# Optimization experiments

Measured on AMD Instinct MI355X. Metric: run time of the kernel, lower is better.

## Reference

```python
import jax, jax.numpy as jnp
import numpy as np

B, T, H, D = 4, 1024, 16, 64


def setup_inputs() -> dict:
    key = jax.random.key(0)
    kq, kk, kwq, kwk = jax.random.split(key, 4)
    q = jax.random.normal(kq, (B, T, H, D), dtype=jnp.float32)
    k = jax.random.normal(kk, (B, T, H, D), dtype=jnp.float32)
    # HedgehogFeatureMap init: eye weight, zero bias; add small noise so grads flow
    Wq = jnp.eye(D, dtype=jnp.float32) + 0.02 * jax.random.normal(kwq, (D, D), dtype=jnp.float32)
    Wk = jnp.eye(D, dtype=jnp.float32) + 0.02 * jax.random.normal(kwk, (D, D), dtype=jnp.float32)
    bq = jnp.zeros((D,), dtype=jnp.float32)
    bk = jnp.zeros((D,), dtype=jnp.float32)
    return {"q": q, "k": k, "Wq": Wq, "bq": bq, "Wk": Wk, "bk": bk}


def _feature_map(x, W, b):
    # nn.Linear(head_dim, head_dim) then cat([exp(y), exp(-y)], -1) -> [..., 2D]
    y = jnp.einsum('bthd,ed->bthe', x, W) + b
    return jnp.concatenate([jnp.exp(y), jnp.exp(-y)], axis=-1)


def reference(q, k, Wq, bq, Wk, bk):
    # true softmax attention map: [B, T, H, T]
    scale = q.shape[-1] ** 0.5
    scores = jnp.einsum('bthd,bThd->bthT', q, k) / scale
    true_attn_map = jax.nn.softmax(scores, axis=-1)
    # predicted quadratic linear attention with hedgehog feature maps
    phi_q = _feature_map(q, Wq, bq)   # [B,T,H,2D]
    phi_k = _feature_map(k, Wk, bk)   # [B,T,H,2D]
    qk = jnp.einsum('bthd,bThd->bthT', phi_q, phi_k)
    pred_attn_map = qk / jnp.sum(qk, axis=-1, keepdims=True)
    return jnp.stack([true_attn_map, pred_attn_map])  # [2,B,T,H,T]
```

## Files before the change

### kernel.cpp

```cpp
#include <hip/hip_runtime.h>

typedef unsigned short u16;
typedef unsigned int u32;
typedef __attribute__((ext_vector_type(8))) short short8;
typedef __attribute__((ext_vector_type(4))) float floatx4;

#define MFMA16(A,B,C) __builtin_amdgcn_mfma_f32_16x16x32_bf16((A),(B),(C),0,0,0)


__device__ __forceinline__ u16 f2bf(float f){
  u32 u = __float_as_uint(f);
  u32 r = (u + 0x7fffu + ((u >> 16) & 1u)) >> 16;
  return (u16)r;
}
__device__ __forceinline__ float bf2f(u16 h){
  return __uint_as_float(((u32)h) << 16);
}
__device__ __forceinline__ short8 ld8(const u16* p){
  return *(const short8*)p;
}

__global__ __launch_bounds__(256) void featmap_kernel(
    const float* __restrict__ q, const float* __restrict__ k,
    const float* __restrict__ Wq, const float* __restrict__ bq,
    const float* __restrict__ Wk, const float* __restrict__ bk,
    u16* __restrict__ qh, u16* __restrict__ ql,
    u16* __restrict__ kh, u16* __restrict__ kl,
    u16* __restrict__ phiq, u16* __restrict__ phik) {
  u32 gid = blockIdx.x * 256u + threadIdx.x;
  bool is_k = gid >= 65536u;
  u32 r = is_k ? (gid - 65536u) : gid;
  const float* __restrict__ x = (is_k ? k : q) + (size_t)r * 64u;
  const float* __restrict__ W = is_k ? Wk : Wq;
  const float* __restrict__ bias = is_k ? bk : bq;
  u32 b = r >> 14, t = (r >> 4) & 1023u, h = r & 15u;
  u32 orow = (b * 16u + h) * 1024u + t;

  float xv[64];
#pragma unroll
  for (int i = 0; i < 16; i++) {
    float4 v = ((const float4*)x)[i];
    xv[4 * i + 0] = v.x; xv[4 * i + 1] = v.y;
    xv[4 * i + 2] = v.z; xv[4 * i + 3] = v.w;
  }

  float scale = is_k ? 1.0f : 0.125f;
  u16* hdst = (is_k ? kh : qh) + (size_t)orow * 64u;
  u16* ldst = (is_k ? kl : ql) + (size_t)orow * 64u;
#pragma unroll
  for (int c = 0; c < 8; c++) {
    u16 hi[8] __attribute__((aligned(16)));
    u16 lo[8] __attribute__((aligned(16)));
#pragma unroll
    for (int j = 0; j < 8; j++) {
      float xs = xv[c * 8 + j] * scale;
      u16 hb = f2bf(xs);
      hi[j] = hb;
      lo[j] = f2bf(xs - bf2f(hb));
    }
    ((uint4*)hdst)[c] = *(const uint4*)hi;
    ((uint4*)ldst)[c] = *(const uint4*)lo;
  }

  u16* pdst = (is_k ? phik : phiq) + (size_t)orow * 128u;
#pragma unroll
  for (int c = 0; c < 4; c++) {
    float accs[16];
#pragma unroll
    for (int i = 0; i < 16; i++) accs[i] = bias[c * 16 + i];
#pragma unroll
    for (int d = 0; d < 64; d++) {
      float xd = xv[d];
#pragma unroll
      for (int i = 0; i < 16; i++) accs[i] += xd * W[(c * 16 + i) * 64 + d];
    }
    u16 pl[16] __attribute__((aligned(16)));
    u16 pm[16] __attribute__((aligned(16)));
#pragma unroll
    for (int i = 0; i < 16; i++) {
      pl[i] = f2bf(__expf(accs[i]));
      pm[i] = f2bf(__expf(-accs[i]));
    }
    ((uint4*)pdst)[2 * c + 0] = ((const uint4*)pl)[0];
    ((uint4*)pdst)[2 * c + 1] = ((const uint4*)pl)[1];
    ((uint4*)(pdst + 64))[2 * c + 0] = ((const uint4*)pm)[0];
    ((uint4*)(pdst + 64))[2 * c + 1] = ((const uint4*)pm)[1];
  }
}

__global__ __launch_bounds__(128) void colsum_kernel(
    const u16* __restrict__ phik, float* __restrict__ colsum) {
  int bh = blockIdx.x;
  int e = threadIdx.x;
  const u16* p = phik + (size_t)bh * 1024u * 128u + e;
  float s = 0.f;
#pragma unroll 8
  for (int t = 0; t < 1024; t++) s += bf2f(p[(size_t)t * 128u]);
  colsum[bh * 128 + e] = s;
}

__global__ __launch_bounds__(256) void fused_kernel(
    const u16* __restrict__ qh, const u16* __restrict__ ql,
    const u16* __restrict__ kh, const u16* __restrict__ kl,
    const u16* __restrict__ phiq, const u16* __restrict__ phik,
    const float* __restrict__ colsum, float* __restrict__ out) {
  int bh = blockIdx.x >> 6, strip = blockIdx.x & 63;
  int tid = threadIdx.x, w = tid >> 6, lane = tid & 63, quad = lane >> 4, n16 = lane & 15;
  u32 base = (u32)bh * 1024u;

  __shared__ float cs[128];
  __shared__ float rzp_s[16];
  __shared__ float zb[4][16];

  if (tid < 128) cs[tid] = colsum[bh * 128 + tid];
  __syncthreads();

  {
    int row = tid >> 4, seg = tid & 15;
    u32 grow = base + strip * 16u + (u32)row;
    short8 v = ld8(phiq + (size_t)grow * 128u + seg * 8);
    float p = 0.f;
#pragma unroll
    for (int j = 0; j < 8; j++) p += bf2f((u16)v[j]) * cs[seg * 8 + j];
#pragma unroll
    for (int off = 1; off < 16; off <<= 1) p += __shfl_xor(p, off);
    if (seg == 0) rzp_s[row] = 1.f / p;
  }

  u32 qrow = base + strip * 16u + n16;
  short8 bqh[2], bql[2], bpq[4];
#pragma unroll
  for (int ks = 0; ks < 2; ks++) {
    bqh[ks] = ld8(qh + (size_t)qrow * 64u + ks * 32u + quad * 8u);
    bql[ks] = ld8(ql + (size_t)qrow * 64u + ks * 32u + quad * 8u);
  }
#pragma unroll
  for (int ks = 0; ks < 4; ks++)
    bpq[ks] = ld8(phiq + (size_t)qrow * 128u + ks * 32u + quad * 8u);

  __syncthreads();
  float rzp = rzp_s[n16];

  u32 bb = (u32)bh >> 4, hh = (u32)bh & 15u;
  u32 t = strip * 16u + n16;
  float* out0 = out + ((size_t)(bb * 1024u + t) * 16u + hh) * 1024u;
  float* out1 = out0 + 67108864u;

  float pt[64];
#pragma unroll
  for (int ct = 0; ct < 16; ct++) {
    u32 col = base + (u32)(w * 16 + ct) * 16u + n16;
    const u16* kp = kh + (size_t)col * 64u + quad * 8u;
    const u16* lp = kl + (size_t)col * 64u + quad * 8u;
    const u16* pp = phik + (size_t)col * 128u + quad * 8u;
    short8 b0 = ld8(kp), b1 = ld8(kp + 32), c0 = ld8(lp), c1 = ld8(lp + 32);
    short8 p0 = ld8(pp), p1 = ld8(pp + 32), p2 = ld8(pp + 64), p3 = ld8(pp + 96);
    floatx4 acc = {0.f, 0.f, 0.f, 0.f};
    acc = MFMA16(b0, bqh[0], acc);
    acc = MFMA16(b1, bqh[1], acc);
    acc = MFMA16(c0, bqh[0], acc);
    acc = MFMA16(c1, bqh[1], acc);
    acc = MFMA16(b0, bql[0], acc);
    acc = MFMA16(b1, bql[1], acc);
    floatx4 ap = {0.f, 0.f, 0.f, 0.f};
    ap = MFMA16(p0, bpq[0], ap);
    ap = MFMA16(p1, bpq[1], ap);
    ap = MFMA16(p2, bpq[2], ap);
    ap = MFMA16(p3, bpq[3], ap);
#pragma unroll
    for (int r = 0; r < 4; r++) pt[ct * 4 + r] = __expf(acc[r]);
    float4 ov;
    ov.x = ap[0] * rzp; ov.y = ap[1] * rzp;
    ov.z = ap[2] * rzp; ov.w = ap[3] * rzp;
    *(float4*)(out1 + (u32)(w * 16 + ct) * 16u + quad * 4u) = ov;
  }

  float s = 0.f;
#pragma unroll
  for (int i = 0; i < 64; i++) s += pt[i];
  s += __shfl_xor(s, 16);
  s += __shfl_xor(s, 32);
  if (lane < 16) zb[w][lane] = s;
  __syncthreads();
  float rzt = 1.f / (zb[0][n16] + zb[1][n16] + zb[2][n16] + zb[3][n16]);

#pragma unroll
  for (int ct = 0; ct < 16; ct++) {
    float4 ov;
    ov.x = pt[ct * 4 + 0] * rzt; ov.y = pt[ct * 4 + 1] * rzt;
    ov.z = pt[ct * 4 + 2] * rzt; ov.w = pt[ct * 4 + 3] * rzt;
    *(float4*)(out0 + (u32)(w * 16 + ct) * 16u + quad * 4u) = ov;
  }
}

extern "C" void kernel_launch(void* const* d_in, const int* in_sizes, int n_in,
                              void* d_out, int out_size, void* d_ws, size_t ws_size,
                              hipStream_t stream) {
  const float* q  = (const float*)d_in[0];
  const float* k  = (const float*)d_in[1];
  const float* Wq = (const float*)d_in[2];
  const float* bq = (const float*)d_in[3];
  const float* Wk = (const float*)d_in[4];
  const float* bk = (const float*)d_in[5];
  unsigned char* ws = (unsigned char*)d_ws;
  u16* qh   = (u16*)(ws + (0ull  << 20));
  u16* ql   = (u16*)(ws + (8ull  << 20));
  u16* kh   = (u16*)(ws + (16ull << 20));
  u16* kl   = (u16*)(ws + (24ull << 20));
  u16* phiq = (u16*)(ws + (32ull << 20));
  u16* phik = (u16*)(ws + (48ull << 20));
  float* colsum = (float*)(ws + (64ull << 20));
  float* out = (float*)d_out;

  hipLaunchKernelGGL(featmap_kernel, dim3(512), dim3(256), 0, stream,
                     q, k, Wq, bq, Wk, bk, qh, ql, kh, kl, phiq, phik);
  hipLaunchKernelGGL(colsum_kernel, dim3(64), dim3(128), 0, stream, phik, colsum);
  hipLaunchKernelGGL(fused_kernel, dim3(4096), dim3(256), 0, stream,
                     qh, ql, kh, kl, phiq, phik, colsum, out);
}
```

Measured before the change: 937.6 us.

## Widen fused blocks to 16 waves, split colsum with atomics, remap featmap rows

The fused kernel now runs 1024 threads per block, so each of 16 waves covers 4 column tiles instead of 16. This shrinks per-thread register arrays and spreads the row-softmax reduction over 16 waves. The colsum reduction is split across 8 chunks per head, combined with atomicAdd, with featmap zeroing the accumulator first. Featmap threads are remapped so consecutive threads write consecutive output rows rather than consecutive input rows. This trades strided input reads for contiguous workspace writes, and the larger blocks may lower occupancy flexibility.

```diff
diff --git a/kernel.cpp b/kernel.cpp
--- a/kernel.cpp
+++ b/kernel.cpp
@@ -26,15 +26,19 @@
     const float* __restrict__ Wk, const float* __restrict__ bk,
     u16* __restrict__ qh, u16* __restrict__ ql,
     u16* __restrict__ kh, u16* __restrict__ kl,
-    u16* __restrict__ phiq, u16* __restrict__ phik) {
+    u16* __restrict__ phiq, u16* __restrict__ phik,
+    float* __restrict__ colsum) {
   u32 gid = blockIdx.x * 256u + threadIdx.x;
+  if (gid < 8192u) colsum[gid] = 0.f;
   bool is_k = gid >= 65536u;
   u32 r = is_k ? (gid - 65536u) : gid;
-  const float* __restrict__ x = (is_k ? k : q) + (size_t)r * 64u;
+  u32 t = r & 1023u, bh = r >> 10;
+  u32 b = bh >> 4, h = bh & 15u;
+  const float* __restrict__ x =
+      (is_k ? k : q) + ((size_t)(b * 1024u + t) * 16u + h) * 64u;
   const float* __restrict__ W = is_k ? Wk : Wq;
   const float* __restrict__ bias = is_k ? bk : bq;
-  u32 b = r >> 14, t = (r >> 4) & 1023u, h = r & 15u;
-  u32 orow = (b * 16u + h) * 1024u + t;
+  u32 orow = bh * 1024u + t;
 
   float xv[64];
 #pragma unroll
@@ -90,16 +94,16 @@
 
 __global__ __launch_bounds__(128) void colsum_kernel(
     const u16* __restrict__ phik, float* __restrict__ colsum) {
-  int bh = blockIdx.x;
+  int bh = blockIdx.x >> 3, chunk = blockIdx.x & 7;
   int e = threadIdx.x;
-  const u16* p = phik + (size_t)bh * 1024u * 128u + e;
+  const u16* p = phik + (size_t)bh * 131072u + (size_t)chunk * 16384u + e;
   float s = 0.f;
 #pragma unroll 8
-  for (int t = 0; t < 1024; t++) s += bf2f(p[(size_t)t * 128u]);
-  colsum[bh * 128 + e] = s;
-}
-
-__global__ __launch_bounds__(256) void fused_kernel(
+  for (int t = 0; t < 128; t++) s += bf2f(p[(size_t)t * 128u]);
+  atomicAdd(&colsum[bh * 128 + e], s);
+}
+
+__global__ __launch_bounds__(1024) void fused_kernel(
     const u16* __restrict__ qh, const u16* __restrict__ ql,
     const u16* __restrict__ kh, const u16* __restrict__ kl,
     const u16* __restrict__ phiq, const u16* __restrict__ phik,
@@ -110,12 +114,12 @@
 
   __shared__ float cs[128];
   __shared__ float rzp_s[16];
-  __shared__ float zb[4][16];
+  __shared__ float zb[16][16];
 
   if (tid < 128) cs[tid] = colsum[bh * 128 + tid];
   __syncthreads();
 
-  {
+  if (tid < 256) {
     int row = tid >> 4, seg = tid & 15;
     u32 grow = base + strip * 16u + (u32)row;
     short8 v = ld8(phiq + (size_t)grow * 128u + seg * 8);
@@ -146,10 +150,11 @@
   float* out0 = out + ((size_t)(bb * 1024u + t) * 16u + hh) * 1024u;
   float* out1 = out0 + 67108864u;
 
-  float pt[64];
-#pragma unroll
-  for (int ct = 0; ct < 16; ct++) {
-    u32 col = base + (u32)(w * 16 + ct) * 16u + n16;
+  float pt[16];
+#pragma unroll
+  for (int ct = 0; ct < 4; ct++) {
+    u32 ctg = (u32)(w * 4 + ct);
+    u32 col = base + ctg * 16u + n16;
     const u16* kp = kh + (size_t)col * 64u + quad * 8u;
     const u16* lp = kl + (size_t)col * 64u + quad * 8u;
     const u16* pp = phik + (size_t)col * 128u + quad * 8u;
@@ -172,24 +177,28 @@
     float4 ov;
     ov.x = ap[0] * rzp; ov.y = ap[1] * rzp;
     ov.z = ap[2] * rzp; ov.w = ap[3] * rzp;
-    *(float4*)(out1 + (u32)(w * 16 + ct) * 16u + quad * 4u) = ov;
+    *(float4*)(out1 + ctg * 16u + quad * 4u) = ov;
   }
 
   float s = 0.f;
 #pragma unroll
-  for (int i = 0; i < 64; i++) s += pt[i];
+  for (int i = 0; i < 16; i++) s += pt[i];
   s += __shfl_xor(s, 16);
   s += __shfl_xor(s, 32);
   if (lane < 16) zb[w][lane] = s;
   __syncthreads();
-  float rzt = 1.f / (zb[0][n16] + zb[1][n16] + zb[2][n16] + zb[3][n16]);
-
-#pragma unroll
-  for (int ct = 0; ct < 16; ct++) {
+  float zt = 0.f;
+#pragma unroll
+  for (int w2 = 0; w2 < 16; w2++) zt += zb[w2][n16];
+  float rzt = 1.f / zt;
+
+#pragma unroll
+  for (int ct = 0; ct < 4; ct++) {
+    u32 ctg = (u32)(w * 4 + ct);
     float4 ov;
     ov.x = pt[ct * 4 + 0] * rzt; ov.y = pt[ct * 4 + 1] * rzt;
     ov.z = pt[ct * 4 + 2] * rzt; ov.w = pt[ct * 4 + 3] * rzt;
-    *(float4*)(out0 + (u32)(w * 16 + ct) * 16u + quad * 4u) = ov;
+    *(float4*)(out0 + ctg * 16u + quad * 4u) = ov;
   }
 }
 
@@ -213,8 +222,8 @@
   float* out = (float*)d_out;
 
   hipLaunchKernelGGL(featmap_kernel, dim3(512), dim3(256), 0, stream,
-                     q, k, Wq, bq, Wk, bk, qh, ql, kh, kl, phiq, phik);
-  hipLaunchKernelGGL(colsum_kernel, dim3(64), dim3(128), 0, stream, phik, colsum);
-  hipLaunchKernelGGL(fused_kernel, dim3(4096), dim3(256), 0, stream,
+                     q, k, Wq, bq, Wk, bk, qh, ql, kh, kl, phiq, phik, colsum);
+  hipLaunchKernelGGL(colsum_kernel, dim3(512), dim3(128), 0, stream, phik, colsum);
+  hipLaunchKernelGGL(fused_kernel, dim3(4096), dim3(1024), 0, stream,
                      qh, ql, kh, kl, phiq, phik, colsum, out);
 }
```

Result: no change. 936.5 us (-0.1%).

## Stage attention tiles in LDS for coalesced row writes and drop colsum kernel

Applied to the files above, without the earlier changes.

The feature-map kernel now writes intermediates in the original [B,T,H] row order instead of a permuted head-major layout. The fused kernel grows to 1024 threads and stages both score tiles (16 rows by 1024 cols) in shared memory. Each wave then reads a full row, reduces it with wave shuffles, and writes contiguous 4KB output rows. The separate colsum pass and its prediction denominator are replaced by a direct row-sum of the predicted scores. The cost is about 128KB of LDS per block, which limits occupancy to one block per CU, and the K/phi reads become strided because of the unpermuted layout.

```diff
diff --git a/kernel.cpp b/kernel.cpp
--- a/kernel.cpp
+++ b/kernel.cpp
@@ -33,8 +33,6 @@
   const float* __restrict__ x = (is_k ? k : q) + (size_t)r * 64u;
   const float* __restrict__ W = is_k ? Wk : Wq;
   const float* __restrict__ bias = is_k ? bk : bq;
-  u32 b = r >> 14, t = (r >> 4) & 1023u, h = r & 15u;
-  u32 orow = (b * 16u + h) * 1024u + t;
 
   float xv[64];
 #pragma unroll
@@ -45,8 +43,8 @@
   }
 
   float scale = is_k ? 1.0f : 0.125f;
-  u16* hdst = (is_k ? kh : qh) + (size_t)orow * 64u;
-  u16* ldst = (is_k ? kl : ql) + (size_t)orow * 64u;
+  u16* hdst = (is_k ? kh : qh) + (size_t)r * 64u;
+  u16* ldst = (is_k ? kl : ql) + (size_t)r * 64u;
 #pragma unroll
   for (int c = 0; c < 8; c++) {
     u16 hi[8] __attribute__((aligned(16)));
@@ -62,7 +60,7 @@
     ((uint4*)ldst)[c] = *(const uint4*)lo;
   }
 
-  u16* pdst = (is_k ? phik : phiq) + (size_t)orow * 128u;
+  u16* pdst = (is_k ? phik : phiq) + (size_t)r * 128u;
 #pragma unroll
   for (int c = 0; c < 4; c++) {
     float accs[16];
@@ -88,71 +86,38 @@
   }
 }
 
-__global__ __launch_bounds__(128) void colsum_kernel(
-    const u16* __restrict__ phik, float* __restrict__ colsum) {
-  int bh = blockIdx.x;
-  int e = threadIdx.x;
-  const u16* p = phik + (size_t)bh * 1024u * 128u + e;
-  float s = 0.f;
-#pragma unroll 8
-  for (int t = 0; t < 1024; t++) s += bf2f(p[(size_t)t * 128u]);
-  colsum[bh * 128 + e] = s;
-}
-
-__global__ __launch_bounds__(256) void fused_kernel(
+__global__ __launch_bounds__(1024) void fused_kernel(
     const u16* __restrict__ qh, const u16* __restrict__ ql,
     const u16* __restrict__ kh, const u16* __restrict__ kl,
     const u16* __restrict__ phiq, const u16* __restrict__ phik,
-    const float* __restrict__ colsum, float* __restrict__ out) {
+    float* __restrict__ out) {
   int bh = blockIdx.x >> 6, strip = blockIdx.x & 63;
   int tid = threadIdx.x, w = tid >> 6, lane = tid & 63, quad = lane >> 4, n16 = lane & 15;
-  u32 base = (u32)bh * 1024u;
-
-  __shared__ float cs[128];
-  __shared__ float rzp_s[16];
-  __shared__ float zb[4][16];
-
-  if (tid < 128) cs[tid] = colsum[bh * 128 + tid];
-  __syncthreads();
-
-  {
-    int row = tid >> 4, seg = tid & 15;
-    u32 grow = base + strip * 16u + (u32)row;
-    short8 v = ld8(phiq + (size_t)grow * 128u + seg * 8);
-    float p = 0.f;
-#pragma unroll
-    for (int j = 0; j < 8; j++) p += bf2f((u16)v[j]) * cs[seg * 8 + j];
-#pragma unroll
-    for (int off = 1; off < 16; off <<= 1) p += __shfl_xor(p, off);
-    if (seg == 0) rzp_s[row] = 1.f / p;
-  }
-
-  u32 qrow = base + strip * 16u + n16;
+  u32 b = (u32)bh >> 4, h = (u32)bh & 15u;
+
+  __shared__ float smT[16][1028];
+  __shared__ float smP[16][1028];
+
+  u32 tq = (u32)strip * 16u + (u32)n16;
+  size_t Rq = (size_t)((b * 1024u + tq) * 16u + h);
   short8 bqh[2], bql[2], bpq[4];
 #pragma unroll
   for (int ks = 0; ks < 2; ks++) {
-    bqh[ks] = ld8(qh + (size_t)qrow * 64u + ks * 32u + quad * 8u);
-    bql[ks] = ld8(ql + (size_t)qrow * 64u + ks * 32u + quad * 8u);
+    bqh[ks] = ld8(qh + Rq * 64u + ks * 32 + quad * 8);
+    bql[ks] = ld8(ql + Rq * 64u + ks * 32 + quad * 8);
   }
 #pragma unroll
   for (int ks = 0; ks < 4; ks++)
-    bpq[ks] = ld8(phiq + (size_t)qrow * 128u + ks * 32u + quad * 8u);
-
-  __syncthreads();
-  float rzp = rzp_s[n16];
-
-  u32 bb = (u32)bh >> 4, hh = (u32)bh & 15u;
-  u32 t = strip * 16u + n16;
-  float* out0 = out + ((size_t)(bb * 1024u + t) * 16u + hh) * 1024u;
-  float* out1 = out0 + 67108864u;
-
-  float pt[64];
-#pragma unroll
-  for (int ct = 0; ct < 16; ct++) {
-    u32 col = base + (u32)(w * 16 + ct) * 16u + n16;
-    const u16* kp = kh + (size_t)col * 64u + quad * 8u;
-    const u16* lp = kl + (size_t)col * 64u + quad * 8u;
-    const u16* pp = phik + (size_t)col * 128u + quad * 8u;
+    bpq[ks] = ld8(phiq + Rq * 128u + ks * 32 + quad * 8);
+
+#pragma unroll
+  for (int ct = 0; ct < 4; ct++) {
+    u32 ctg = (u32)(w * 4 + ct);
+    u32 tk = ctg * 16u + (u32)n16;
+    size_t Rk = (size_t)((b * 1024u + tk) * 16u + h);
+    const u16* kp = kh + Rk * 64u + quad * 8;
+    const u16* lp = kl + Rk * 64u + quad * 8;
+    const u16* pp = phik + Rk * 128u + quad * 8;
     short8 b0 = ld8(kp), b1 = ld8(kp + 32), c0 = ld8(lp), c1 = ld8(lp + 32);
     short8 p0 = ld8(pp), p1 = ld8(pp + 32), p2 = ld8(pp + 64), p3 = ld8(pp + 96);
     floatx4 acc = {0.f, 0.f, 0.f, 0.f};
@@ -167,29 +132,48 @@
     ap = MFMA16(p1, bpq[1], ap);
     ap = MFMA16(p2, bpq[2], ap);
     ap = MFMA16(p3, bpq[3], ap);
-#pragma unroll
-    for (int r = 0; r < 4; r++) pt[ct * 4 + r] = __expf(acc[r]);
+    float4 tv;
+    tv.x = __expf(acc[0]); tv.y = __expf(acc[1]);
+    tv.z = __expf(acc[2]); tv.w = __expf(acc[3]);
+    float4 pv;
+    pv.x = ap[0]; pv.y = ap[1]; pv.z = ap[2]; pv.w = ap[3];
+    *(float4*)&smT[n16][ctg * 16u + quad * 4u] = tv;
+    *(float4*)&smP[n16][ctg * 16u + quad * 4u] = pv;
+  }
+  __syncthreads();
+
+  float4 tv[4], pv[4];
+#pragma unroll
+  for (int j = 0; j < 4; j++) {
+    tv[j] = *(const float4*)&smT[w][j * 256 + lane * 4];
+    pv[j] = *(const float4*)&smP[w][j * 256 + lane * 4];
+  }
+  float st = 0.f, sp = 0.f;
+#pragma unroll
+  for (int j = 0; j < 4; j++) {
+    st += tv[j].x + tv[j].y + tv[j].z + tv[j].w;
+    sp += pv[j].x + pv[j].y + pv[j].z + pv[j].w;
+  }
+#pragma unroll
+  for (int off = 1; off < 64; off <<= 1) {
+    st += __shfl_xor(st, off);
+    sp += __shfl_xor(sp, off);
+  }
+  float rzt = 1.f / st, rzp = 1.f / sp;
+
+  u32 tr = (u32)strip * 16u + (u32)w;
+  float* out0 = out + (size_t)((b * 1024u + tr) * 16u + h) * 1024u;
+  float* out1 = out0 + 67108864u;
+#pragma unroll
+  for (int j = 0; j < 4; j++) {
     float4 ov;
-    ov.x = ap[0] * rzp; ov.y = ap[1] * rzp;
-    ov.z = ap[2] * rzp; ov.w = ap[3] * rzp;
-    *(float4*)(out1 + (u32)(w * 16 + ct) * 16u + quad * 4u) = ov;
-  }
-
-  float s = 0.f;
-#pragma unroll
-  for (int i = 0; i < 64; i++) s += pt[i];
-  s += __shfl_xor(s, 16);
-  s += __shfl_xor(s, 32);
-  if (lane < 16) zb[w][lane] = s;
-  __syncthreads();
-  float rzt = 1.f / (zb[0][n16] + zb[1][n16] + zb[2][n16] + zb[3][n16]);
-
-#pragma unroll
-  for (int ct = 0; ct < 16; ct++) {
-    float4 ov;
-    ov.x = pt[ct * 4 + 0] * rzt; ov.y = pt[ct * 4 + 1] * rzt;
-    ov.z = pt[ct * 4 + 2] * rzt; ov.w = pt[ct * 4 + 3] * rzt;
-    *(float4*)(out0 + (u32)(w * 16 + ct) * 16u + quad * 4u) = ov;
+    ov.x = tv[j].x * rzt; ov.y = tv[j].y * rzt;
+    ov.z = tv[j].z * rzt; ov.w = tv[j].w * rzt;
+    *(float4*)(out0 + j * 256 + lane * 4) = ov;
+    float4 pw;
+    pw.x = pv[j].x * rzp; pw.y = pv[j].y * rzp;
+    pw.z = pv[j].z * rzp; pw.w = pv[j].w * rzp;
+    *(float4*)(out1 + j * 256 + lane * 4) = pw;
   }
 }
 
@@ -209,12 +193,10 @@
   u16* kl   = (u16*)(ws + (24ull << 20));
   u16* phiq = (u16*)(ws + (32ull << 20));
   u16* phik = (u16*)(ws + (48ull << 20));
-  float* colsum = (float*)(ws + (64ull << 20));
   float* out = (float*)d_out;
 
   hipLaunchKernelGGL(featmap_kernel, dim3(512), dim3(256), 0, stream,
                      q, k, Wq, bq, Wk, bk, qh, ql, kh, kl, phiq, phik);
-  hipLaunchKernelGGL(colsum_kernel, dim3(64), dim3(128), 0, stream, phik, colsum);
-  hipLaunchKernelGGL(fused_kernel, dim3(4096), dim3(256), 0, stream,
-                     qh, ql, kh, kl, phiq, phik, colsum, out);
-}
+  hipLaunchKernelGGL(fused_kernel, dim3(4096), dim3(1024), 0, stream,
+                     qh, ql, kh, kl, phiq, phik, out);
+}
```

Measured after the change: 939.3 us. No clear change (+0.2%).
